# Performance work log

Hardware: AMD Instinct MI355X
Metric: run time of the kernel (lower is better)

## Reference

```python
import jax, jax.numpy as jnp
import numpy as np

HIDDEN = 4096
N_EXPERTS = 128
TOP_K = 8
N_GROUP = 8
TOPK_GROUP = 4
ROUTED_SCALE = 1.0
NORM_TOPK = True
T = 32768


def setup_inputs() -> dict:
    key = jax.random.key(0)
    k1, k2, k3 = jax.random.split(key, 3)
    hidden_states = jax.random.normal(k1, (T, HIDDEN), dtype=jnp.float32)
    weight = jax.random.normal(k2, (N_EXPERTS, HIDDEN), dtype=jnp.float32) * 0.02
    e_score_correction_bias = jax.random.normal(k3, (N_EXPERTS,), dtype=jnp.float32) * 0.1
    return {"hidden_states": hidden_states, "weight": weight,
            "e_score_correction_bias": e_score_correction_bias}


def reference(hidden_states, weight, e_score_correction_bias):
    # GLM4-MoE top-k router: linear -> sigmoid -> bias-corrected grouped top-k
    x = hidden_states.reshape(-1, HIDDEN)
    router_logits = jnp.einsum('th,eh->te', x, weight)          # [T, E]
    scores = jax.nn.sigmoid(router_logits)                      # [T, E]
    scores_for_choice = scores + e_score_correction_bias[None, :]

    per_group = N_EXPERTS // N_GROUP
    g = scores_for_choice.reshape(-1, N_GROUP, per_group)       # [T, G, E/G]
    # group score = sum of top-2 expert scores within each group
    group_scores = jax.lax.top_k(g, 2)[0].sum(axis=-1)          # [T, G]
    group_idx = jax.lax.top_k(group_scores, TOPK_GROUP)[1]      # [T, topk_group]
    group_mask = jax.nn.one_hot(group_idx, N_GROUP, dtype=scores.dtype).sum(axis=1)  # [T, G]
    score_mask = jnp.repeat(group_mask, per_group, axis=-1)     # [T, E]
    masked_scores = jnp.where(score_mask > 0, scores_for_choice, 0.0)

    topk_indices = jax.lax.top_k(masked_scores, TOP_K)[1]       # [T, top_k]
    topk_weights = jnp.take_along_axis(scores, topk_indices, axis=1)  # gather raw (un-biased) scores
    if NORM_TOPK:
        denom = topk_weights.sum(axis=-1, keepdims=True) + 1e-20
        topk_weights = topk_weights / denom
    topk_weights = topk_weights * ROUTED_SCALE
    return topk_indices, topk_weights
```

## Files before the change

### kernel.cpp

```cpp
#include <hip/hip_runtime.h>
#include <math.h>

#define T_TOKENS 32768
#define HIDDEN   4096
#define NEXP     128
#define TM       64
#define BK       32
#define NSTAGE   (HIDDEN / BK)

#define A_BUF_SH      6144
#define B_BASE_SH     (2 * A_BUF_SH)
#define B_BUF_SH      12288
#define LDS_SHORTS    (B_BASE_SH + 2 * B_BUF_SH)
#define B_BASE_BYTES  (B_BASE_SH * 2)
#define B_BUF_BYTES   (B_BUF_SH * 2)
#define A_PLANE_SH    2048
#define B_PLANE_SH    4096
#define SC_STRIDE     129
#define B_CHUNK_BYTES B_BUF_BYTES
#define WS_BYTES ((size_t)NSTAGE * B_CHUNK_BYTES)

typedef short bf16x8 __attribute__((ext_vector_type(8)));
typedef short bf16x4 __attribute__((ext_vector_type(4)));
typedef float f32x4  __attribute__((ext_vector_type(4)));

__device__ __forceinline__ unsigned short f2bf(float f) {
    unsigned u = __float_as_uint(f);
    u += 0x7FFF + ((u >> 16) & 1);
    return (unsigned short)(u >> 16);
}
__device__ __forceinline__ float bf2f(unsigned short h) {
    return __uint_as_float(((unsigned)h) << 16);
}
__device__ __forceinline__ void split3(float x, unsigned short& b0,
                                       unsigned short& b1, unsigned short& b2) {
    b0 = f2bf(x);
    float r1 = x - bf2f(b0);
    b1 = f2bf(r1);
    float r2 = r1 - bf2f(b1);
    b2 = f2bf(r2);
}

__global__ __launch_bounds__(256) void presplit_w(
    const float* __restrict__ w, short* __restrict__ ws16)
{
    const int g = blockIdx.x * 256 + threadIdx.x;
    const int l = g & 63;
    const int t = (g >> 6) & 7;
    const int s = g >> 9;
    const int e  = t * 16 + (l & 15);
    const int kb = s * BK + ((l >> 4) & 3) * 8;
    const float* src = w + (size_t)e * HIDDEN + kb;
    float4 v0 = *(const float4*)(src);
    float4 v1 = *(const float4*)(src + 4);
    float vv[8] = {v0.x, v0.y, v0.z, v0.w, v1.x, v1.y, v1.z, v1.w};
    unsigned short h0[8], h1[8], h2[8];
#pragma unroll
    for (int j = 0; j < 8; ++j) split3(vv[j], h0[j], h1[j], h2[j]);
    const size_t base = ((size_t)s * 24 + t) * 64 + l;
    bf16x8 o0 = {(short)h0[0],(short)h0[1],(short)h0[2],(short)h0[3],
                 (short)h0[4],(short)h0[5],(short)h0[6],(short)h0[7]};
    bf16x8 o1 = {(short)h1[0],(short)h1[1],(short)h1[2],(short)h1[3],
                 (short)h1[4],(short)h1[5],(short)h1[6],(short)h1[7]};
    bf16x8 o2 = {(short)h2[0],(short)h2[1],(short)h2[2],(short)h2[3],
                 (short)h2[4],(short)h2[5],(short)h2[6],(short)h2[7]};
    *(bf16x8*)(ws16 + (base + 0 * 8 * 64) * 8) = o0;
    *(bf16x8*)(ws16 + (base + 1 * 8 * 64) * 8) = o1;
    *(bf16x8*)(ws16 + (base + 2 * 8 * 64) * 8) = o2;
}

__global__ __launch_bounds__(512, 4) void glm4_router_mfma(
    const float* __restrict__ x, const short* __restrict__ wsplit,
    const float* __restrict__ bias, float* __restrict__ out)
{
    __shared__ __align__(16) short lds[LDS_SHORTS];

    const int tid  = threadIdx.x;
    const int wid  = tid >> 6;
    const int lane = tid & 63;
    const int rt_base = (wid & 1) * 2;
    const int ct_base = (wid >> 1) * 2;
    const int tok_base = blockIdx.x * TM;

    const int al = (tid >> 1) & 63;
    const int at = tid >> 7;
    const int arow = at * 16 + (al & 15);
    const int akoff = ((al >> 4) & 3) * 8 + (tid & 1) * 4;
    const float* xsrc = x + (size_t)(tok_base + arow) * HIDDEN + akoff;
    const int awr = tid * 4;

    f32x4 acc[2][2];
    double accd[2][2][4];
#pragma unroll
    for (int r = 0; r < 2; ++r)
#pragma unroll
        for (int c = 0; c < 2; ++c) {
            acc[r][c] = (f32x4){0.f, 0.f, 0.f, 0.f};
#pragma unroll
            for (int v = 0; v < 4; ++v) accd[r][c][v] = 0.0;
        }

#define GLDS_B(S, BUF) do {                                                    \
    const char* gsrc_ = (const char*)wsplit + (size_t)(S) * B_CHUNK_BYTES + tid * 16; \
    char* ldst_ = (char*)lds + B_BASE_BYTES + (BUF) * B_BUF_BYTES + tid * 16;  \
    __builtin_amdgcn_global_load_lds(                                          \
        (const __attribute__((address_space(1))) unsigned*)(gsrc_),            \
        (__attribute__((address_space(3))) unsigned*)(ldst_), 16, 0, 0);       \
    __builtin_amdgcn_global_load_lds(                                          \
        (const __attribute__((address_space(1))) unsigned*)(gsrc_ + 8192),     \
        (__attribute__((address_space(3))) unsigned*)(ldst_ + 8192), 16, 0, 0);\
    __builtin_amdgcn_global_load_lds(                                          \
        (const __attribute__((address_space(1))) unsigned*)(gsrc_ + 16384),    \
        (__attribute__((address_space(3))) unsigned*)(ldst_ + 16384), 16, 0, 0);\
} while (0)

#define SPLIT_A(XV, BUF) do {                                                  \
    unsigned short h0_[4], h1_[4], h2_[4];                                     \
    split3((XV).x, h0_[0], h1_[0], h2_[0]);                                    \
    split3((XV).y, h0_[1], h1_[1], h2_[1]);                                    \
    split3((XV).z, h0_[2], h1_[2], h2_[2]);                                    \
    split3((XV).w, h0_[3], h1_[3], h2_[3]);                                    \
    short* ab_ = &lds[(BUF) * A_BUF_SH + awr];                                 \
    *(bf16x4*)(ab_ + 0 * A_PLANE_SH) =                                         \
        (bf16x4){(short)h0_[0], (short)h0_[1], (short)h0_[2], (short)h0_[3]};  \
    *(bf16x4*)(ab_ + 1 * A_PLANE_SH) =                                         \
        (bf16x4){(short)h1_[0], (short)h1_[1], (short)h1_[2], (short)h1_[3]};  \
    *(bf16x4*)(ab_ + 2 * A_PLANE_SH) =                                         \
        (bf16x4){(short)h2_[0], (short)h2_[1], (short)h2_[2], (short)h2_[3]};  \
} while (0)

#define MFMA_COL(C, B0_, B1_, B2_) do {                                        \
    _Pragma("unroll")                                                          \
    for (int r = 0; r < 2; ++r) {                                              \
        acc[r][C] = __builtin_amdgcn_mfma_f32_16x16x32_bf16(Af[0][r], B0_, acc[r][C], 0, 0, 0); \
        acc[r][C] = __builtin_amdgcn_mfma_f32_16x16x32_bf16(Af[0][r], B1_, acc[r][C], 0, 0, 0); \
        acc[r][C] = __builtin_amdgcn_mfma_f32_16x16x32_bf16(Af[1][r], B0_, acc[r][C], 0, 0, 0); \
        acc[r][C] = __builtin_amdgcn_mfma_f32_16x16x32_bf16(Af[0][r], B2_, acc[r][C], 0, 0, 0); \
        acc[r][C] = __builtin_amdgcn_mfma_f32_16x16x32_bf16(Af[2][r], B0_, acc[r][C], 0, 0, 0); \
        acc[r][C] = __builtin_amdgcn_mfma_f32_16x16x32_bf16(Af[1][r], B1_, acc[r][C], 0, 0, 0); \
    }                                                                          \
} while (0)

#define BODY(S, BUF, XC, XL) do {                                              \
    GLDS_B((S) + 1, (BUF) ^ 1);                                                \
    {                                                                          \
        int s2_ = (S) + 2; if (s2_ > NSTAGE - 1) s2_ = NSTAGE - 1;             \
        XL = *(const float4*)(xsrc + (size_t)s2_ * BK);                        \
    }                                                                          \
    bf16x8 Af[3][2];                                                           \
    _Pragma("unroll")                                                          \
    for (int p = 0; p < 3; ++p)                                                \
        _Pragma("unroll")                                                      \
        for (int r = 0; r < 2; ++r)                                            \
            Af[p][r] = *(const bf16x8*)(&lds[(BUF) * A_BUF_SH + p * A_PLANE_SH \
                                             + ((rt_base + r) * 64 + lane) * 8]); \
    {                                                                          \
        bf16x8 Bc0 = *(const bf16x8*)(&lds[B_BASE_SH + (BUF) * B_BUF_SH        \
                          + 0 * B_PLANE_SH + ((ct_base + 0) * 64 + lane) * 8]);\
        bf16x8 Bc1 = *(const bf16x8*)(&lds[B_BASE_SH + (BUF) * B_BUF_SH        \
                          + 1 * B_PLANE_SH + ((ct_base + 0) * 64 + lane) * 8]);\
        bf16x8 Bc2 = *(const bf16x8*)(&lds[B_BASE_SH + (BUF) * B_BUF_SH        \
                          + 2 * B_PLANE_SH + ((ct_base + 0) * 64 + lane) * 8]);\
        __builtin_amdgcn_s_setprio(1);                                         \
        MFMA_COL(0, Bc0, Bc1, Bc2);                                            \
        __builtin_amdgcn_s_setprio(0);                                         \
    }                                                                          \
    SPLIT_A(XC, (BUF) ^ 1);         \
    {                                                                          \
        bf16x8 Bc0 = *(const bf16x8*)(&lds[B_BASE_SH + (BUF) * B_BUF_SH        \
                          + 0 * B_PLANE_SH + ((ct_base + 1) * 64 + lane) * 8]);\
        bf16x8 Bc1 = *(const bf16x8*)(&lds[B_BASE_SH + (BUF) * B_BUF_SH        \
                          + 1 * B_PLANE_SH + ((ct_base + 1) * 64 + lane) * 8]);\
        bf16x8 Bc2 = *(const bf16x8*)(&lds[B_BASE_SH + (BUF) * B_BUF_SH        \
                          + 2 * B_PLANE_SH + ((ct_base + 1) * 64 + lane) * 8]);\
        __builtin_amdgcn_s_setprio(1);                                         \
        MFMA_COL(1, Bc0, Bc1, Bc2);                                            \
        __builtin_amdgcn_s_setprio(0);                                         \
    }                                                                          \
    if (((S) & 3) == 3) {                                                      \
        _Pragma("unroll")                                                      \
        for (int r = 0; r < 2; ++r)                                            \
            _Pragma("unroll")                                                  \
            for (int c = 0; c < 2; ++c) {                                      \
                _Pragma("unroll")                                              \
                for (int v = 0; v < 4; ++v) accd[r][c][v] += (double)acc[r][c][v]; \
                acc[r][c] = (f32x4){0.f, 0.f, 0.f, 0.f};                       \
            }                                                                  \
    }                                                                          \
    __syncthreads();       \
} while (0)

    float4 xA, xB;
    {
        float4 x0v = *(const float4*)(xsrc);
        GLDS_B(0, 0);
        xA = *(const float4*)(xsrc + BK);
        SPLIT_A(x0v, 0);
    }
    __syncthreads();

    for (int s = 0; s < NSTAGE - 2; s += 2) {
        BODY(s, 0, xA, xB);
        BODY(s + 1, 1, xB, xA);
    }
    BODY(NSTAGE - 2, 0, xA, xB);

    {
        bf16x8 Af[3][2];
#pragma unroll
        for (int p = 0; p < 3; ++p)
#pragma unroll
            for (int r = 0; r < 2; ++r)
                Af[p][r] = *(const bf16x8*)(&lds[1 * A_BUF_SH + p * A_PLANE_SH
                                                 + ((rt_base + r) * 64 + lane) * 8]);
#pragma unroll
        for (int c = 0; c < 2; ++c) {
            bf16x8 Bc0 = *(const bf16x8*)(&lds[B_BASE_SH + 1 * B_BUF_SH
                              + 0 * B_PLANE_SH + ((ct_base + c) * 64 + lane) * 8]);
            bf16x8 Bc1 = *(const bf16x8*)(&lds[B_BASE_SH + 1 * B_BUF_SH
                              + 1 * B_PLANE_SH + ((ct_base + c) * 64 + lane) * 8]);
            bf16x8 Bc2 = *(const bf16x8*)(&lds[B_BASE_SH + 1 * B_BUF_SH
                              + 2 * B_PLANE_SH + ((ct_base + c) * 64 + lane) * 8]);
#pragma unroll
            for (int r = 0; r < 2; ++r) {
                acc[r][c] = __builtin_amdgcn_mfma_f32_16x16x32_bf16(Af[0][r], Bc0, acc[r][c], 0, 0, 0);
                acc[r][c] = __builtin_amdgcn_mfma_f32_16x16x32_bf16(Af[0][r], Bc1, acc[r][c], 0, 0, 0);
                acc[r][c] = __builtin_amdgcn_mfma_f32_16x16x32_bf16(Af[1][r], Bc0, acc[r][c], 0, 0, 0);
                acc[r][c] = __builtin_amdgcn_mfma_f32_16x16x32_bf16(Af[0][r], Bc2, acc[r][c], 0, 0, 0);
                acc[r][c] = __builtin_amdgcn_mfma_f32_16x16x32_bf16(Af[2][r], Bc0, acc[r][c], 0, 0, 0);
                acc[r][c] = __builtin_amdgcn_mfma_f32_16x16x32_bf16(Af[1][r], Bc1, acc[r][c], 0, 0, 0);
            }
        }
#pragma unroll
        for (int r = 0; r < 2; ++r)
#pragma unroll
            for (int c = 0; c < 2; ++c)
#pragma unroll
                for (int v = 0; v < 4; ++v) accd[r][c][v] += (double)acc[r][c][v];
    }

    __syncthreads();
    float* sc = (float*)lds;
#pragma unroll
    for (int r = 0; r < 2; ++r)
#pragma unroll
        for (int c = 0; c < 2; ++c) {
#pragma unroll
            for (int v = 0; v < 4; ++v) {
                const int tokl = (rt_base + r) * 16 + (lane >> 4) * 4 + v;
                const int e    = (ct_base + c) * 16 + (lane & 15);
                const float lg = (float)accd[r][c][v];
                const float sg = (float)(1.0 / (1.0 + exp(-(double)lg)));
                sc[tokl * SC_STRIDE + e] = sg + bias[e];
            }
        }
    __syncthreads();

    if (tid < TM) {
        const float* scp = sc + tid * SC_STRIDE;

        float gsc[8];
#pragma unroll
        for (int g = 0; g < 8; ++g) {
            float m1 = -1e30f, m2 = -1e30f;
#pragma unroll
            for (int j = 0; j < 16; ++j) {
                const float v = scp[g * 16 + j];
                if (v > m1) { m2 = m1; m1 = v; }
                else if (v > m2) { m2 = v; }
            }
            gsc[g] = m1 + m2;
        }

        unsigned gmask = 0;
#pragma unroll
        for (int p = 0; p < 4; ++p) {
            float best = -1e30f; int bi = 0;
#pragma unroll
            for (int g = 0; g < 8; ++g) {
                const bool taken = (gmask >> g) & 1u;
                if (!taken && gsc[g] > best) { best = gsc[g]; bi = g; }
            }
            gmask |= 1u << bi;
        }

        unsigned long long chosen0 = 0ull, chosen1 = 0ull;
        int   idxs[8];
        float wts[8];
#pragma unroll
        for (int p = 0; p < 8; ++p) {
            float best = -1e30f; int bi = 0;
            for (int e = 0; e < NEXP; ++e) {
                const bool sel = (gmask >> (e >> 4)) & 1u;
                const float v = sel ? scp[e] : 0.0f;
                const bool ch = (e < 64) ? ((chosen0 >> e) & 1ull)
                                         : ((chosen1 >> (e - 64)) & 1ull);
                if (!ch && v > best) { best = v; bi = e; }
            }
            if (bi < 64) chosen0 |= 1ull << bi; else chosen1 |= 1ull << (bi - 64);
            idxs[p] = bi;
            wts[p] = scp[bi] - bias[bi];
        }

        float denom = 0.0f;
#pragma unroll
        for (int p = 0; p < 8; ++p) denom += wts[p];
        denom += 1e-20f;

        const size_t row = (size_t)(tok_base + tid) * 8;
        float* outI = out;
        float* outW = out + (size_t)T_TOKENS * 8;
#pragma unroll
        for (int p = 0; p < 8; ++p) {
            outI[row + p] = (float)idxs[p];
            outW[row + p] = wts[p] / denom;
        }
    }
}

extern "C" void kernel_launch(void* const* d_in, const int* in_sizes, int n_in,
                              void* d_out, int out_size, void* d_ws, size_t ws_size,
                              hipStream_t stream) {
    const float* x    = (const float*)d_in[0];
    const float* w    = (const float*)d_in[1];
    const float* bias = (const float*)d_in[2];
    float* out = (float*)d_out;
    short* ws16 = (short*)d_ws;

    presplit_w<<<dim3(NSTAGE * 8 * 64 / 256), 256, 0, stream>>>(w, ws16);
    glm4_router_mfma<<<dim3(T_TOKENS / TM), 512, 0, stream>>>(x, ws16, bias, out);
}
```

Baseline: 274.5 us.

## Replace 3-way bf16 split GEMM with 2-way scaled fp16 split

Switches the fp32-emulating matmul from a three-plane bf16 decomposition (6 MFMAs per tile) to a two-plane fp16 decomposition with the residual scaled by 4096 (3 MFMAs per tile), accumulated in separate main and correction accumulators. This halves MFMA count and cuts LDS and weight-workspace traffic by a third. The scaled fp16 residual with flushing of subnormal high parts may lose precision for small or large magnitudes, which could flip near-tie top-k selections.

```diff
diff --git a/kernel.cpp b/kernel.cpp
--- a/kernel.cpp
+++ b/kernel.cpp
@@ -8,41 +8,32 @@
 #define BK       32
 #define NSTAGE   (HIDDEN / BK)
 
-#define A_BUF_SH      6144
+#define A_PLANE_SH    2048
+#define A_BUF_SH      (2 * A_PLANE_SH)
 #define B_BASE_SH     (2 * A_BUF_SH)
-#define B_BUF_SH      12288
+#define B_PLANE_SH    4096
+#define B_BUF_SH      (2 * B_PLANE_SH)
 #define LDS_SHORTS    (B_BASE_SH + 2 * B_BUF_SH)
 #define B_BASE_BYTES  (B_BASE_SH * 2)
 #define B_BUF_BYTES   (B_BUF_SH * 2)
-#define A_PLANE_SH    2048
-#define B_PLANE_SH    4096
 #define SC_STRIDE     129
 #define B_CHUNK_BYTES B_BUF_BYTES
 #define WS_BYTES ((size_t)NSTAGE * B_CHUNK_BYTES)
 
-typedef short bf16x8 __attribute__((ext_vector_type(8)));
-typedef short bf16x4 __attribute__((ext_vector_type(4)));
+typedef _Float16 f16x8 __attribute__((ext_vector_type(8)));
+typedef _Float16 f16x4 __attribute__((ext_vector_type(4)));
 typedef float f32x4  __attribute__((ext_vector_type(4)));
 
-__device__ __forceinline__ unsigned short f2bf(float f) {
-    unsigned u = __float_as_uint(f);
-    u += 0x7FFF + ((u >> 16) & 1);
-    return (unsigned short)(u >> 16);
+__device__ __forceinline__ void split2(float x, _Float16& h0, _Float16& h1) {
+    _Float16 a = (_Float16)x;
+    float af = (float)a;
+    if (__builtin_fabsf(af) < 6.103515625e-05f) { a = (_Float16)0.0f; af = 0.0f; }
+    h0 = a;
+    h1 = (_Float16)((x - af) * 4096.0f);
 }
-__device__ __forceinline__ float bf2f(unsigned short h) {
-    return __uint_as_float(((unsigned)h) << 16);
-}
-__device__ __forceinline__ void split3(float x, unsigned short& b0,
-                                       unsigned short& b1, unsigned short& b2) {
-    b0 = f2bf(x);
-    float r1 = x - bf2f(b0);
-    b1 = f2bf(r1);
-    float r2 = r1 - bf2f(b1);
-    b2 = f2bf(r2);
-}
 
 __global__ __launch_bounds__(256) void presplit_w(
-    const float* __restrict__ w, short* __restrict__ ws16)
+    const float* __restrict__ w, _Float16* __restrict__ ws16)
 {
     const int g = blockIdx.x * 256 + threadIdx.x;
     const int l = g & 63;
@@ -54,26 +45,19 @@
     float4 v0 = *(const float4*)(src);
     float4 v1 = *(const float4*)(src + 4);
     float vv[8] = {v0.x, v0.y, v0.z, v0.w, v1.x, v1.y, v1.z, v1.w};
-    unsigned short h0[8], h1[8], h2[8];
-#pragma unroll
-    for (int j = 0; j < 8; ++j) split3(vv[j], h0[j], h1[j], h2[j]);
-    const size_t base = ((size_t)s * 24 + t) * 64 + l;
-    bf16x8 o0 = {(short)h0[0],(short)h0[1],(short)h0[2],(short)h0[3],
-                 (short)h0[4],(short)h0[5],(short)h0[6],(short)h0[7]};
-    bf16x8 o1 = {(short)h1[0],(short)h1[1],(short)h1[2],(short)h1[3],
-                 (short)h1[4],(short)h1[5],(short)h1[6],(short)h1[7]};
-    bf16x8 o2 = {(short)h2[0],(short)h2[1],(short)h2[2],(short)h2[3],
-                 (short)h2[4],(short)h2[5],(short)h2[6],(short)h2[7]};
-    *(bf16x8*)(ws16 + (base + 0 * 8 * 64) * 8) = o0;
-    *(bf16x8*)(ws16 + (base + 1 * 8 * 64) * 8) = o1;
-    *(bf16x8*)(ws16 + (base + 2 * 8 * 64) * 8) = o2;
+    _Float16 h0[8], h1[8];
+#pragma unroll
+    for (int j = 0; j < 8; ++j) split2(vv[j], h0[j], h1[j]);
+    _Float16* dst = ws16 + (size_t)s * 8192 + (t * 64 + l) * 8;
+    *(f16x8*)(dst)        = (f16x8){h0[0],h0[1],h0[2],h0[3],h0[4],h0[5],h0[6],h0[7]};
+    *(f16x8*)(dst + 4096) = (f16x8){h1[0],h1[1],h1[2],h1[3],h1[4],h1[5],h1[6],h1[7]};
 }
 
 __global__ __launch_bounds__(512, 4) void glm4_router_mfma(
-    const float* __restrict__ x, const short* __restrict__ wsplit,
+    const float* __restrict__ x, const _Float16* __restrict__ wsplit,
     const float* __restrict__ bias, float* __restrict__ out)
 {
-    __shared__ __align__(16) short lds[LDS_SHORTS];
+    __shared__ __align__(16) _Float16 lds[LDS_SHORTS];
 
     const int tid  = threadIdx.x;
     const int wid  = tid >> 6;
@@ -89,13 +73,15 @@
     const float* xsrc = x + (size_t)(tok_base + arow) * HIDDEN + akoff;
     const int awr = tid * 4;
 
-    f32x4 acc[2][2];
+    f32x4 mainA[2][2];
+    f32x4 corr[2][2];
     double accd[2][2][4];
 #pragma unroll
     for (int r = 0; r < 2; ++r)
 #pragma unroll
         for (int c = 0; c < 2; ++c) {
-            acc[r][c] = (f32x4){0.f, 0.f, 0.f, 0.f};
+            mainA[r][c] = (f32x4){0.f, 0.f, 0.f, 0.f};
+            corr[r][c]  = (f32x4){0.f, 0.f, 0.f, 0.f};
 #pragma unroll
             for (int v = 0; v < 4; ++v) accd[r][c][v] = 0.0;
         }
@@ -109,35 +95,25 @@
     __builtin_amdgcn_global_load_lds(                                          \
         (const __attribute__((address_space(1))) unsigned*)(gsrc_ + 8192),     \
         (__attribute__((address_space(3))) unsigned*)(ldst_ + 8192), 16, 0, 0);\
-    __builtin_amdgcn_global_load_lds(                                          \
-        (const __attribute__((address_space(1))) unsigned*)(gsrc_ + 16384),    \
-        (__attribute__((address_space(3))) unsigned*)(ldst_ + 16384), 16, 0, 0);\
 } while (0)
 
 #define SPLIT_A(XV, BUF) do {                                                  \
-    unsigned short h0_[4], h1_[4], h2_[4];                                     \
-    split3((XV).x, h0_[0], h1_[0], h2_[0]);                                    \
-    split3((XV).y, h0_[1], h1_[1], h2_[1]);                                    \
-    split3((XV).z, h0_[2], h1_[2], h2_[2]);                                    \
-    split3((XV).w, h0_[3], h1_[3], h2_[3]);                                    \
-    short* ab_ = &lds[(BUF) * A_BUF_SH + awr];                                 \
-    *(bf16x4*)(ab_ + 0 * A_PLANE_SH) =                                         \
-        (bf16x4){(short)h0_[0], (short)h0_[1], (short)h0_[2], (short)h0_[3]};  \
-    *(bf16x4*)(ab_ + 1 * A_PLANE_SH) =                                         \
-        (bf16x4){(short)h1_[0], (short)h1_[1], (short)h1_[2], (short)h1_[3]};  \
-    *(bf16x4*)(ab_ + 2 * A_PLANE_SH) =                                         \
-        (bf16x4){(short)h2_[0], (short)h2_[1], (short)h2_[2], (short)h2_[3]};  \
+    _Float16 h0_[4], h1_[4];                                                   \
+    split2((XV).x, h0_[0], h1_[0]);                                            \
+    split2((XV).y, h0_[1], h1_[1]);                                            \
+    split2((XV).z, h0_[2], h1_[2]);                                            \
+    split2((XV).w, h0_[3], h1_[3]);                                            \
+    _Float16* ab_ = &lds[(BUF) * A_BUF_SH + awr];                              \
+    *(f16x4*)(ab_)              = (f16x4){h0_[0], h0_[1], h0_[2], h0_[3]};     \
+    *(f16x4*)(ab_ + A_PLANE_SH) = (f16x4){h1_[0], h1_[1], h1_[2], h1_[3]};     \
 } while (0)
 
-#define MFMA_COL(C, B0_, B1_, B2_) do {                                        \
+#define MFMA_COL(C, B0_, B1_) do {                                             \
     _Pragma("unroll")                                                          \
     for (int r = 0; r < 2; ++r) {                                              \
-        acc[r][C] = __builtin_amdgcn_mfma_f32_16x16x32_bf16(Af[0][r], B0_, acc[r][C], 0, 0, 0); \
-        acc[r][C] = __builtin_amdgcn_mfma_f32_16x16x32_bf16(Af[0][r], B1_, acc[r][C], 0, 0, 0); \
-        acc[r][C] = __builtin_amdgcn_mfma_f32_16x16x32_bf16(Af[1][r], B0_, acc[r][C], 0, 0, 0); \
-        acc[r][C] = __builtin_amdgcn_mfma_f32_16x16x32_bf16(Af[0][r], B2_, acc[r][C], 0, 0, 0); \
-        acc[r][C] = __builtin_amdgcn_mfma_f32_16x16x32_bf16(Af[2][r], B0_, acc[r][C], 0, 0, 0); \
-        acc[r][C] = __builtin_amdgcn_mfma_f32_16x16x32_bf16(Af[1][r], B1_, acc[r][C], 0, 0, 0); \
+        mainA[r][C] = __builtin_amdgcn_mfma_f32_16x16x32_f16(Af0[r], B0_, mainA[r][C], 0, 0, 0); \
+        corr[r][C]  = __builtin_amdgcn_mfma_f32_16x16x32_f16(Af0[r], B1_, corr[r][C], 0, 0, 0);  \
+        corr[r][C]  = __builtin_amdgcn_mfma_f32_16x16x32_f16(Af1[r], B0_, corr[r][C], 0, 0, 0);  \
     }                                                                          \
 } while (0)
 
@@ -147,34 +123,31 @@
         int s2_ = (S) + 2; if (s2_ > NSTAGE - 1) s2_ = NSTAGE - 1;             \
         XL = *(const float4*)(xsrc + (size_t)s2_ * BK);                        \
     }                                                                          \
-    bf16x8 Af[3][2];                                                           \
+    f16x8 Af0[2], Af1[2];                                                      \
     _Pragma("unroll")                                                          \
-    for (int p = 0; p < 3; ++p)                                                \
-        _Pragma("unroll")                                                      \
-        for (int r = 0; r < 2; ++r)                                            \
-            Af[p][r] = *(const bf16x8*)(&lds[(BUF) * A_BUF_SH + p * A_PLANE_SH \
-                                             + ((rt_base + r) * 64 + lane) * 8]); \
+    for (int r = 0; r < 2; ++r) {                                              \
+        Af0[r] = *(const f16x8*)(&lds[(BUF) * A_BUF_SH                         \
+                                      + ((rt_base + r) * 64 + lane) * 8]);     \
+        Af1[r] = *(const f16x8*)(&lds[(BUF) * A_BUF_SH + A_PLANE_SH            \
+                                      + ((rt_base + r) * 64 + lane) * 8]);     \
+    }                                                                          \
     {                                                                          \
-        bf16x8 Bc0 = *(const bf16x8*)(&lds[B_BASE_SH + (BUF) * B_BUF_SH        \
-                          + 0 * B_PLANE_SH + ((ct_base + 0) * 64 + lane) * 8]);\
-        bf16x8 Bc1 = *(const bf16x8*)(&lds[B_BASE_SH + (BUF) * B_BUF_SH        \
-                          + 1 * B_PLANE_SH + ((ct_base + 0) * 64 + lane) * 8]);\
-        bf16x8 Bc2 = *(const bf16x8*)(&lds[B_BASE_SH + (BUF) * B_BUF_SH        \
-                          + 2 * B_PLANE_SH + ((ct_base + 0) * 64 + lane) * 8]);\
+        f16x8 B0_ = *(const f16x8*)(&lds[B_BASE_SH + (BUF) * B_BUF_SH          \
+                          + ((ct_base + 0) * 64 + lane) * 8]);                 \
+        f16x8 B1_ = *(const f16x8*)(&lds[B_BASE_SH + (BUF) * B_BUF_SH          \
+                          + B_PLANE_SH + ((ct_base + 0) * 64 + lane) * 8]);    \
         __builtin_amdgcn_s_setprio(1);                                         \
-        MFMA_COL(0, Bc0, Bc1, Bc2);                                            \
+        MFMA_COL(0, B0_, B1_);                                                 \
         __builtin_amdgcn_s_setprio(0);                                         \
     }                                                                          \
     SPLIT_A(XC, (BUF) ^ 1);         \
     {                                                                          \
-        bf16x8 Bc0 = *(const bf16x8*)(&lds[B_BASE_SH + (BUF) * B_BUF_SH        \
-                          + 0 * B_PLANE_SH + ((ct_base + 1) * 64 + lane) * 8]);\
-        bf16x8 Bc1 = *(const bf16x8*)(&lds[B_BASE_SH + (BUF) * B_BUF_SH        \
-                          + 1 * B_PLANE_SH + ((ct_base + 1) * 64 + lane) * 8]);\
-        bf16x8 Bc2 = *(const bf16x8*)(&lds[B_BASE_SH + (BUF) * B_BUF_SH        \
-                          + 2 * B_PLANE_SH + ((ct_base + 1) * 64 + lane) * 8]);\
+        f16x8 B0_ = *(const f16x8*)(&lds[B_BASE_SH + (BUF) * B_BUF_SH          \
+                          + ((ct_base + 1) * 64 + lane) * 8]);                 \
+        f16x8 B1_ = *(const f16x8*)(&lds[B_BASE_SH + (BUF) * B_BUF_SH          \
+                          + B_PLANE_SH + ((ct_base + 1) * 64 + lane) * 8]);    \
         __builtin_amdgcn_s_setprio(1);                                         \
-        MFMA_COL(1, Bc0, Bc1, Bc2);                                            \
+        MFMA_COL(1, B0_, B1_);                                                 \
         __builtin_amdgcn_s_setprio(0);                                         \
     }                                                                          \
     if (((S) & 3) == 3) {                                                      \
@@ -183,8 +156,11 @@
             _Pragma("unroll")                                                  \
             for (int c = 0; c < 2; ++c) {                                      \
                 _Pragma("unroll")                                              \
-                for (int v = 0; v < 4; ++v) accd[r][c][v] += (double)acc[r][c][v]; \
-                acc[r][c] = (f32x4){0.f, 0.f, 0.f, 0.f};                       \
+                for (int v = 0; v < 4; ++v)                                    \
+                    accd[r][c][v] += (double)mainA[r][c][v]                    \
+                                   + (double)corr[r][c][v] * (1.0 / 4096.0);   \
+                mainA[r][c] = (f32x4){0.f, 0.f, 0.f, 0.f};                     \
+                corr[r][c]  = (f32x4){0.f, 0.f, 0.f, 0.f};                     \
             }                                                                  \
     }                                                                          \
     __syncthreads();       \
@@ -206,29 +182,25 @@
     BODY(NSTAGE - 2, 0, xA, xB);
 
     {
-        bf16x8 Af[3][2];
-#pragma unroll
-        for (int p = 0; p < 3; ++p)
-#pragma unroll
-            for (int r = 0; r < 2; ++r)
-                Af[p][r] = *(const bf16x8*)(&lds[1 * A_BUF_SH + p * A_PLANE_SH
-                                                 + ((rt_base + r) * 64 + lane) * 8]);
+        f16x8 Af0[2], Af1[2];
+#pragma unroll
+        for (int r = 0; r < 2; ++r) {
+            Af0[r] = *(const f16x8*)(&lds[1 * A_BUF_SH
+                                          + ((rt_base + r) * 64 + lane) * 8]);
+            Af1[r] = *(const f16x8*)(&lds[1 * A_BUF_SH + A_PLANE_SH
+                                          + ((rt_base + r) * 64 + lane) * 8]);
+        }
 #pragma unroll
         for (int c = 0; c < 2; ++c) {
-            bf16x8 Bc0 = *(const bf16x8*)(&lds[B_BASE_SH + 1 * B_BUF_SH
-                              + 0 * B_PLANE_SH + ((ct_base + c) * 64 + lane) * 8]);
-            bf16x8 Bc1 = *(const bf16x8*)(&lds[B_BASE_SH + 1 * B_BUF_SH
-                              + 1 * B_PLANE_SH + ((ct_base + c) * 64 + lane) * 8]);
-            bf16x8 Bc2 = *(const bf16x8*)(&lds[B_BASE_SH + 1 * B_BUF_SH
-                              + 2 * B_PLANE_SH + ((ct_base + c) * 64 + lane) * 8]);
+            f16x8 B0_ = *(const f16x8*)(&lds[B_BASE_SH + 1 * B_BUF_SH
+                              + ((ct_base + c) * 64 + lane) * 8]);
+            f16x8 B1_ = *(const f16x8*)(&lds[B_BASE_SH + 1 * B_BUF_SH
+                              + B_PLANE_SH + ((ct_base + c) * 64 + lane) * 8]);
 #pragma unroll
             for (int r = 0; r < 2; ++r) {
-                acc[r][c] = __builtin_amdgcn_mfma_f32_16x16x32_bf16(Af[0][r], Bc0, acc[r][c], 0, 0, 0);
-                acc[r][c] = __builtin_amdgcn_mfma_f32_16x16x32_bf16(Af[0][r], Bc1, acc[r][c], 0, 0, 0);
-                acc[r][c] = __builtin_amdgcn_mfma_f32_16x16x32_bf16(Af[1][r], Bc0, acc[r][c], 0, 0, 0);
-                acc[r][c] = __builtin_amdgcn_mfma_f32_16x16x32_bf16(Af[0][r], Bc2, acc[r][c], 0, 0, 0);
-                acc[r][c] = __builtin_amdgcn_mfma_f32_16x16x32_bf16(Af[2][r], Bc0, acc[r][c], 0, 0, 0);
-                acc[r][c] = __builtin_amdgcn_mfma_f32_16x16x32_bf16(Af[1][r], Bc1, acc[r][c], 0, 0, 0);
+                mainA[r][c] = __builtin_amdgcn_mfma_f32_16x16x32_f16(Af0[r], B0_, mainA[r][c], 0, 0, 0);
+                corr[r][c]  = __builtin_amdgcn_mfma_f32_16x16x32_f16(Af0[r], B1_, corr[r][c], 0, 0, 0);
+                corr[r][c]  = __builtin_amdgcn_mfma_f32_16x16x32_f16(Af1[r], B0_, corr[r][c], 0, 0, 0);
             }
         }
 #pragma unroll
@@ -236,7 +208,9 @@
 #pragma unroll
             for (int c = 0; c < 2; ++c)
 #pragma unroll
-                for (int v = 0; v < 4; ++v) accd[r][c][v] += (double)acc[r][c][v];
+                for (int v = 0; v < 4; ++v)
+                    accd[r][c][v] += (double)mainA[r][c][v]
+                                   + (double)corr[r][c][v] * (1.0 / 4096.0);
     }
 
     __syncthreads();
@@ -325,7 +299,7 @@
     const float* w    = (const float*)d_in[1];
     const float* bias = (const float*)d_in[2];
     float* out = (float*)d_out;
-    short* ws16 = (short*)d_ws;
+    _Float16* ws16 = (_Float16*)d_ws;
 
     presplit_w<<<dim3(NSTAGE * 8 * 64 / 256), 256, 0, stream>>>(w, ws16);
     glm4_router_mfma<<<dim3(T_TOKENS / TM), 512, 0, stream>>>(x, ws16, bias, out);
```

New measurement: 229.1 us (median of 3 runs). 16.5% less time.
